# Kernel optimization log

Measured on AMD Instinct MI355X. Metric: run time of the kernel, lower is better.

Reference implementation:

```python
import jax, jax.numpy as jnp
import numpy as np

N = 8192
HID = 64
TAU = 0.8
LAMBDA = 0.5
POS_DENSITY = 0.005


def setup_inputs() -> dict:
    key = jax.random.key(0)
    k1, k2, k3, k4, k5, k6, k7 = jax.random.split(key, 7)
    x1 = jax.random.normal(k1, (N, HID), dtype=jnp.float32)
    x2 = jax.random.normal(k2, (N, HID), dtype=jnp.float32)
    # xavier_uniform with gain=1.414 for square [HID, HID] linears
    limit = 1.414 * np.sqrt(6.0 / (HID + HID))
    W1 = jax.random.uniform(k3, (HID, HID), dtype=jnp.float32, minval=-limit, maxval=limit)
    b1 = jnp.zeros((HID,), dtype=jnp.float32)
    W2 = jax.random.uniform(k4, (HID, HID), dtype=jnp.float32, minval=-limit, maxval=limit)
    b2 = jnp.zeros((HID,), dtype=jnp.float32)
    pm = (jax.random.uniform(k5, (N, N), dtype=jnp.float32) < POS_DENSITY).astype(jnp.float32)
    positive_matrix = jnp.maximum(pm, jnp.eye(N, dtype=jnp.float32))
    return {"x1": x1, "x2": x2, "W1": W1, "b1": b1, "W2": W2, "b2": b2,
            "positive_matrix": positive_matrix}


def _project(x, W1, b1, W2, b2):
    # nn.Linear(hidden, hidden) -> ELU -> nn.Linear(hidden, hidden)
    h = jax.nn.elu(x @ W1.T + b1)
    return h @ W2.T + b2


def _l2norm(z, eps=1e-12):
    # F.normalize(p=2, dim=1): x / max(||x||, eps)
    n = jnp.linalg.norm(z, axis=-1, keepdims=True)
    return z / jnp.maximum(n, eps)


def _sim(z1, z2, tau):
    return jnp.exp((_l2norm(z1) @ _l2norm(z2).T) / tau)  # [N, N]


def _masked_loss(sim_mat, pos):
    row = sim_mat / (jnp.sum(sim_mat, axis=-1, keepdims=True) + 1e-8)
    return -jnp.log(jnp.sum(row * pos, axis=-1) + 1e-8).mean()


def reference(x1, x2, W1, b1, W2, b2, positive_matrix):
    z1 = _project(x1, W1, b1, W2, b2)
    z2 = _project(x2, W1, b1, W2, b2)
    sc_mp = _sim(z1, z2, TAU)
    mp_sc = _sim(z2, z1, TAU)
    sc_loss = _masked_loss(sc_mp, positive_matrix)
    mp_loss = _masked_loss(mp_sc, positive_matrix)
    return sc_loss * LAMBDA + mp_loss * (1.0 - LAMBDA)
```

## Files before the change

kernel.cpp:

```cpp
#include <hip/hip_runtime.h>
#include <hip/hip_bf16.h>

#define N 8192
#define HID 64
#define JC 8

typedef __attribute__((ext_vector_type(4))) float f32x4;
typedef __attribute__((ext_vector_type(8))) __bf16 bf16x8;

#if __has_builtin(__builtin_amdgcn_exp2f)
__device__ __forceinline__ float fast_exp2(float x) {
  return __builtin_amdgcn_exp2f(x);
}
#else
__device__ __forceinline__ float fast_exp2(float x) {
  float r;
  asm volatile("v_exp_f32 %0, %1" : "=v"(r) : "v"(x));
  return r;
}
#endif

__device__ __forceinline__ void gload_lds16(const void* g, float* l) {
  __builtin_amdgcn_global_load_lds(
      (const __attribute__((address_space(1))) void*)g,
      (__attribute__((address_space(3))) void*)l, 16, 0, 0);
}

__global__ __launch_bounds__(256) void proj_kernel(
    const float* __restrict__ x1, const float* __restrict__ x2,
    const float* __restrict__ W1, const float* __restrict__ b1,
    const float* __restrict__ W2, const float* __restrict__ b2,
    __bf16* __restrict__ Z1h, __bf16* __restrict__ Z2h,
    float* __restrict__ stats)
{
  __shared__ __align__(16) float w1s[64*68];
  __shared__ __align__(16) float w2s[64*68];
  __shared__ __align__(16) float xs[4][64];
  __shared__ __align__(16) float hs[4][64];

  const int tid  = threadIdx.x;
  const int lane = tid & 63;
  const int w    = tid >> 6;

  int gtid = blockIdx.x * 256 + tid;
  if (gtid < 4*N) stats[gtid] = 0.f;

  for (int idx = tid; idx < 64*64; idx += 256) {
    int j = idx >> 6, k = idx & 63;
    w1s[j*68+k] = W1[idx];
    w2s[j*68+k] = W2[idx];
  }
  __syncthreads();

  const float bias1 = b1[lane];
  const float bias2 = b2[lane];

  const int wave_global = blockIdx.x * 4 + w;
  #pragma unroll 1
  for (int it = 0; it < 4; ++it) {
    int R = wave_global * 4 + it;
    const float* src; __bf16* dst;
    if (R < N) { src = x1 + (size_t)R*HID;      dst = Z1h + (size_t)R*HID; }
    else       { src = x2 + (size_t)(R-N)*HID;  dst = Z2h + (size_t)(R-N)*HID; }

    float xv = src[lane];
    xs[w][lane] = xv;
    float acc = bias1;
    #pragma unroll
    for (int qq = 0; qq < 16; ++qq) {
      f32x4 xq = *(const f32x4*)&xs[w][qq*4];
      f32x4 wq = *(const f32x4*)&w1s[lane*68 + qq*4];
      acc += xq.x*wq.x + xq.y*wq.y + xq.z*wq.z + xq.w*wq.w;
    }
    float h = acc > 0.f ? acc : expm1f(acc);
    hs[w][lane] = h;
    float acc2 = bias2;
    #pragma unroll
    for (int qq = 0; qq < 16; ++qq) {
      f32x4 hq = *(const f32x4*)&hs[w][qq*4];
      f32x4 wq = *(const f32x4*)&w2s[lane*68 + qq*4];
      acc2 += hq.x*wq.x + hq.y*wq.y + hq.z*wq.z + hq.w*wq.w;
    }
    float z = acc2;
    float ss = z*z;
    #pragma unroll
    for (int m = 1; m < 64; m <<= 1) ss += __shfl_xor(ss, m);
    float inv = 1.0f / fmaxf(sqrtf(ss), 1e-12f);
    dst[lane] = (__bf16)(z * inv);
  }
}

__global__ __launch_bounds__(256, 4) void sim_kernel(
    const __bf16* __restrict__ Z1h, const __bf16* __restrict__ Z2h,
    const float* __restrict__ pos,
    float* __restrict__ rowsum1, float* __restrict__ num1,
    float* __restrict__ rowsum2, float* __restrict__ num2)
{
  __shared__ __align__(16) float zs1[2][2048];
  __shared__ __align__(16) float zs2[2][2048];

  const int tid  = threadIdx.x;
  const int lane = tid & 63;
  const int w    = tid >> 6;
  const int r16  = lane & 15;
  const int q    = lane >> 4;

  const int bi  = blockIdx.x / JC;
  const int jc  = blockIdx.x % JC;
  const int i0  = bi*64 + w*16;

  const __bf16* z1r = Z1h + (size_t)(i0 + r16)*HID + q*8;
  const __bf16* z2r = Z2h + (size_t)(i0 + r16)*HID + q*8;
  const bf16x8 a1lo = *(const bf16x8*)(z1r);
  const bf16x8 a1hi = *(const bf16x8*)(z1r + 32);
  const bf16x8 a2lo = *(const bf16x8*)(z2r);
  const bf16x8 a2hi = *(const bf16x8*)(z2r + 32);

  float s1 = 0.f, n1 = 0.f, s2 = 0.f, n2 = 0.f;

  const int jbeg = jc * (N/JC);
  const float Cexp = 1.8033688011112042f;
  const float* prow = pos + (size_t)(i0 + r16)*N + q*4;

  f32x4 PA0, PA1, PA2, PA3, PB0, PB1, PB2, PB3;

#define STAGEZ(BUF, JJ) { \
    const int r8 = lane >> 3; \
    const int sl = (lane & 7) ^ r8; \
    gload_lds16(Z1h + (size_t)((JJ) + w*16     + r8)*HID + sl*8, &zs1[BUF][(w*16    )*32]); \
    gload_lds16(Z1h + (size_t)((JJ) + w*16 + 8 + r8)*HID + sl*8, &zs1[BUF][(w*16 + 8)*32]); \
    gload_lds16(Z2h + (size_t)((JJ) + w*16     + r8)*HID + sl*8, &zs2[BUF][(w*16    )*32]); \
    gload_lds16(Z2h + (size_t)((JJ) + w*16 + 8 + r8)*HID + sl*8, &zs2[BUF][(w*16 + 8)*32]); \
  }

#define LOADPOS(P, JJ) { \
    P##0 = *(const f32x4*)(prow + (JJ)); \
    P##1 = *(const f32x4*)(prow + (JJ) + 16); \
    P##2 = *(const f32x4*)(prow + (JJ) + 32); \
    P##3 = *(const f32x4*)(prow + (JJ) + 48); \
  }

#define COMPC(BUF, C, CC, PV) { \
    const int R  = (CC) + (C)*16 + r16; \
    const int sw = r16 & 7; \
    bf16x8 b2lo = *(const bf16x8*)&zs2[BUF][R*32 + ((q    ) ^ sw)*4]; \
    bf16x8 b2hi = *(const bf16x8*)&zs2[BUF][R*32 + ((q + 4) ^ sw)*4]; \
    bf16x8 b1lo = *(const bf16x8*)&zs1[BUF][R*32 + ((q    ) ^ sw)*4]; \
    bf16x8 b1hi = *(const bf16x8*)&zs1[BUF][R*32 + ((q + 4) ^ sw)*4]; \
    f32x4 zero4 = {0.f,0.f,0.f,0.f}; \
    f32x4 d1 = __builtin_amdgcn_mfma_f32_16x16x32_bf16(b2lo, a1lo, zero4, 0,0,0); \
    d1       = __builtin_amdgcn_mfma_f32_16x16x32_bf16(b2hi, a1hi, d1,    0,0,0); \
    f32x4 d2 = __builtin_amdgcn_mfma_f32_16x16x32_bf16(b1lo, a2lo, zero4, 0,0,0); \
    d2       = __builtin_amdgcn_mfma_f32_16x16x32_bf16(b1hi, a2hi, d2,    0,0,0); \
    _Pragma("unroll") \
    for (int r = 0; r < 4; ++r) { \
      float e1 = fast_exp2(d1[r] * Cexp); \
      float e2 = fast_exp2(d2[r] * Cexp); \
      s1 += e1; n1 += e1 * PV[r]; \
      s2 += e2; n2 += e2 * PV[r]; \
    } }

#define STEP(BUF, P) { COMPC(BUF,0,0,P##0) COMPC(BUF,1,0,P##1) COMPC(BUF,0,32,P##2) COMPC(BUF,1,32,P##3) }

  STAGEZ(0, jbeg)
  LOADPOS(PA, jbeg)
  __syncthreads();

  #pragma unroll 1
  for (int tp = 0; tp < 7; ++tp) {
    const int t0 = tp*2;
    STAGEZ(1, jbeg + (t0+1)*64)
    LOADPOS(PB, jbeg + (t0+1)*64)
    STEP(0, PA)
    __syncthreads();
    STAGEZ(0, jbeg + (t0+2)*64)
    LOADPOS(PA, jbeg + (t0+2)*64)
    STEP(1, PB)
    __syncthreads();
  }
  STAGEZ(1, jbeg + 15*64)
  LOADPOS(PB, jbeg + 15*64)
  STEP(0, PA)
  __syncthreads();
  STEP(1, PB)

#undef STAGEZ
#undef LOADPOS
#undef COMPC
#undef STEP

  s1 += __shfl_xor(s1, 16); s1 += __shfl_xor(s1, 32);
  n1 += __shfl_xor(n1, 16); n1 += __shfl_xor(n1, 32);
  s2 += __shfl_xor(s2, 16); s2 += __shfl_xor(s2, 32);
  n2 += __shfl_xor(n2, 16); n2 += __shfl_xor(n2, 32);

  if (lane < 16) {
    int row = i0 + r16;
    atomicAdd(&rowsum1[row], s1);
    atomicAdd(&num1[row],    n1);
    atomicAdd(&rowsum2[row], s2);
    atomicAdd(&num2[row],    n2);
  }
}

__global__ __launch_bounds__(1024) void loss_kernel(
    const float* __restrict__ rowsum1, const float* __restrict__ num1,
    const float* __restrict__ rowsum2, const float* __restrict__ num2,
    float* __restrict__ out)
{
  __shared__ float part[16];
  const int tid = threadIdx.x, lane = tid & 63, w = tid >> 6;
  float acc = 0.f;
  for (int i = tid; i < N; i += 1024) {
    float sc = -logf(num1[i]/(rowsum1[i]+1e-8f) + 1e-8f);
    float mp = -logf(num2[i]/(rowsum2[i]+1e-8f) + 1e-8f);
    acc += 0.5f*sc + 0.5f*mp;
  }
  #pragma unroll
  for (int m = 1; m < 64; m <<= 1) acc += __shfl_xor(acc, m);
  if (lane == 0) part[w] = acc;
  __syncthreads();
  if (tid == 0) {
    float t = 0.f;
    #pragma unroll
    for (int k = 0; k < 16; ++k) t += part[k];
    out[0] = t * (1.0f/N);
  }
}

extern "C" void kernel_launch(void* const* d_in, const int* in_sizes, int n_in,
                              void* d_out, int out_size, void* d_ws, size_t ws_size,
                              hipStream_t stream) {
  const float* x1  = (const float*)d_in[0];
  const float* x2  = (const float*)d_in[1];
  const float* W1  = (const float*)d_in[2];
  const float* b1  = (const float*)d_in[3];
  const float* W2  = (const float*)d_in[4];
  const float* b2  = (const float*)d_in[5];
  const float* pos = (const float*)d_in[6];

  char* ws = (char*)d_ws;
  __bf16* Z1h = (__bf16*)ws;
  __bf16* Z2h = (__bf16*)(ws + (size_t)N*HID*sizeof(__bf16));
  size_t zbytes = (size_t)2*N*HID*sizeof(__bf16);
  float* rowsum1 = (float*)(ws + zbytes);
  float* num1    = rowsum1 + N;
  float* rowsum2 = num1 + N;
  float* num2    = rowsum2 + N;

  proj_kernel<<<1024, 256, 0, stream>>>(x1, x2, W1, b1, W2, b2, Z1h, Z2h, rowsum1);
  sim_kernel<<<128*JC, 256, 0, stream>>>(Z1h, Z2h, pos, rowsum1, num1, rowsum2, num2);
  loss_kernel<<<1, 1024, 0, stream>>>(rowsum1, num1, rowsum2, num2, (float*)d_out);
}
```

Baseline: 415.8 us.

## Swap sim kernel tiling to stage j-tile once and loop over i-rows

Each block now loads a single 128-column tile of Z1/Z2 into LDS once and iterates over 512 query rows, reloading A fragments and positive-mask rows per iteration. This removes the double-buffered streaming of Z tiles and the per-step barriers. In exchange it drops the software prefetch of the positive mask, so those global loads are exposed each iteration, and it issues more atomic adds per row.

```diff
diff --git a/kernel.cpp b/kernel.cpp
--- a/kernel.cpp
+++ b/kernel.cpp
@@ -3,7 +3,6 @@
 
 #define N 8192
 #define HID 64
-#define JC 8
 
 typedef __attribute__((ext_vector_type(4))) float f32x4;
 typedef __attribute__((ext_vector_type(8))) __bf16 bf16x8;
@@ -96,8 +95,8 @@
     float* __restrict__ rowsum1, float* __restrict__ num1,
     float* __restrict__ rowsum2, float* __restrict__ num2)
 {
-  __shared__ __align__(16) float zs1[2][2048];
-  __shared__ __align__(16) float zs2[2][2048];
+  __shared__ __align__(16) float zs1[128*32];
+  __shared__ __align__(16) float zs2[128*32];
 
   const int tid  = threadIdx.x;
   const int lane = tid & 63;
@@ -105,48 +104,30 @@
   const int r16  = lane & 15;
   const int q    = lane >> 4;
 
-  const int bi  = blockIdx.x / JC;
-  const int jc  = blockIdx.x % JC;
-  const int i0  = bi*64 + w*16;
-
-  const __bf16* z1r = Z1h + (size_t)(i0 + r16)*HID + q*8;
-  const __bf16* z2r = Z2h + (size_t)(i0 + r16)*HID + q*8;
-  const bf16x8 a1lo = *(const bf16x8*)(z1r);
-  const bf16x8 a1hi = *(const bf16x8*)(z1r + 32);
-  const bf16x8 a2lo = *(const bf16x8*)(z2r);
-  const bf16x8 a2hi = *(const bf16x8*)(z2r + 32);
-
-  float s1 = 0.f, n1 = 0.f, s2 = 0.f, n2 = 0.f;
-
-  const int jbeg = jc * (N/JC);
+  const int jb = (blockIdx.x & 63) * 128;
+  const int ig = (blockIdx.x >> 6) * 512;
+
+  {
+    const int r8 = lane >> 3;
+    const int sl = (lane & 7) ^ r8;
+    #pragma unroll
+    for (int b = 0; b < 4; ++b) {
+      const int row0 = w*32 + b*8;
+      gload_lds16(Z1h + (size_t)(jb + row0 + r8)*HID + sl*8, &zs1[row0*32]);
+      gload_lds16(Z2h + (size_t)(jb + row0 + r8)*HID + sl*8, &zs2[row0*32]);
+    }
+  }
+  __syncthreads();
+
   const float Cexp = 1.8033688011112042f;
-  const float* prow = pos + (size_t)(i0 + r16)*N + q*4;
-
-  f32x4 PA0, PA1, PA2, PA3, PB0, PB1, PB2, PB3;
-
-#define STAGEZ(BUF, JJ) { \
-    const int r8 = lane >> 3; \
-    const int sl = (lane & 7) ^ r8; \
-    gload_lds16(Z1h + (size_t)((JJ) + w*16     + r8)*HID + sl*8, &zs1[BUF][(w*16    )*32]); \
-    gload_lds16(Z1h + (size_t)((JJ) + w*16 + 8 + r8)*HID + sl*8, &zs1[BUF][(w*16 + 8)*32]); \
-    gload_lds16(Z2h + (size_t)((JJ) + w*16     + r8)*HID + sl*8, &zs2[BUF][(w*16    )*32]); \
-    gload_lds16(Z2h + (size_t)((JJ) + w*16 + 8 + r8)*HID + sl*8, &zs2[BUF][(w*16 + 8)*32]); \
-  }
-
-#define LOADPOS(P, JJ) { \
-    P##0 = *(const f32x4*)(prow + (JJ)); \
-    P##1 = *(const f32x4*)(prow + (JJ) + 16); \
-    P##2 = *(const f32x4*)(prow + (JJ) + 32); \
-    P##3 = *(const f32x4*)(prow + (JJ) + 48); \
-  }
-
-#define COMPC(BUF, C, CC, PV) { \
-    const int R  = (CC) + (C)*16 + r16; \
+
+#define COMPC(S, PV) { \
+    const int R  = (S)*16 + r16; \
     const int sw = r16 & 7; \
-    bf16x8 b2lo = *(const bf16x8*)&zs2[BUF][R*32 + ((q    ) ^ sw)*4]; \
-    bf16x8 b2hi = *(const bf16x8*)&zs2[BUF][R*32 + ((q + 4) ^ sw)*4]; \
-    bf16x8 b1lo = *(const bf16x8*)&zs1[BUF][R*32 + ((q    ) ^ sw)*4]; \
-    bf16x8 b1hi = *(const bf16x8*)&zs1[BUF][R*32 + ((q + 4) ^ sw)*4]; \
+    bf16x8 b2lo = *(const bf16x8*)&zs2[R*32 + ((q    ) ^ sw)*4]; \
+    bf16x8 b2hi = *(const bf16x8*)&zs2[R*32 + ((q + 4) ^ sw)*4]; \
+    bf16x8 b1lo = *(const bf16x8*)&zs1[R*32 + ((q    ) ^ sw)*4]; \
+    bf16x8 b1hi = *(const bf16x8*)&zs1[R*32 + ((q + 4) ^ sw)*4]; \
     f32x4 zero4 = {0.f,0.f,0.f,0.f}; \
     f32x4 d1 = __builtin_amdgcn_mfma_f32_16x16x32_bf16(b2lo, a1lo, zero4, 0,0,0); \
     d1       = __builtin_amdgcn_mfma_f32_16x16x32_bf16(b2hi, a1hi, d1,    0,0,0); \
@@ -160,47 +141,46 @@
       s2 += e2; n2 += e2 * PV[r]; \
     } }
 
-#define STEP(BUF, P) { COMPC(BUF,0,0,P##0) COMPC(BUF,1,0,P##1) COMPC(BUF,0,32,P##2) COMPC(BUF,1,32,P##3) }
-
-  STAGEZ(0, jbeg)
-  LOADPOS(PA, jbeg)
-  __syncthreads();
-
   #pragma unroll 1
-  for (int tp = 0; tp < 7; ++tp) {
-    const int t0 = tp*2;
-    STAGEZ(1, jbeg + (t0+1)*64)
-    LOADPOS(PB, jbeg + (t0+1)*64)
-    STEP(0, PA)
-    __syncthreads();
-    STAGEZ(0, jbeg + (t0+2)*64)
-    LOADPOS(PA, jbeg + (t0+2)*64)
-    STEP(1, PB)
-    __syncthreads();
-  }
-  STAGEZ(1, jbeg + 15*64)
-  LOADPOS(PB, jbeg + 15*64)
-  STEP(0, PA)
-  __syncthreads();
-  STEP(1, PB)
-
-#undef STAGEZ
-#undef LOADPOS
+  for (int it = 0; it < 8; ++it) {
+    const int i0 = ig + it*64 + w*16;
+
+    const __bf16* z1r = Z1h + (size_t)(i0 + r16)*HID + q*8;
+    const __bf16* z2r = Z2h + (size_t)(i0 + r16)*HID + q*8;
+    const bf16x8 a1lo = *(const bf16x8*)(z1r);
+    const bf16x8 a1hi = *(const bf16x8*)(z1r + 32);
+    const bf16x8 a2lo = *(const bf16x8*)(z2r);
+    const bf16x8 a2hi = *(const bf16x8*)(z2r + 32);
+
+    const float* prow = pos + (size_t)(i0 + r16)*N + jb + q*4;
+    const f32x4 P0 = *(const f32x4*)(prow);
+    const f32x4 P1 = *(const f32x4*)(prow + 16);
+    const f32x4 P2 = *(const f32x4*)(prow + 32);
+    const f32x4 P3 = *(const f32x4*)(prow + 48);
+    const f32x4 P4 = *(const f32x4*)(prow + 64);
+    const f32x4 P5 = *(const f32x4*)(prow + 80);
+    const f32x4 P6 = *(const f32x4*)(prow + 96);
+    const f32x4 P7 = *(const f32x4*)(prow + 112);
+
+    float s1 = 0.f, n1 = 0.f, s2 = 0.f, n2 = 0.f;
+
+    COMPC(0, P0) COMPC(1, P1) COMPC(2, P2) COMPC(3, P3)
+    COMPC(4, P4) COMPC(5, P5) COMPC(6, P6) COMPC(7, P7)
+
+    s1 += __shfl_xor(s1, 16); s1 += __shfl_xor(s1, 32);
+    n1 += __shfl_xor(n1, 16); n1 += __shfl_xor(n1, 32);
+    s2 += __shfl_xor(s2, 16); s2 += __shfl_xor(s2, 32);
+    n2 += __shfl_xor(n2, 16); n2 += __shfl_xor(n2, 32);
+
+    if (lane < 16) {
+      int row = i0 + r16;
+      atomicAdd(&rowsum1[row], s1);
+      atomicAdd(&num1[row],    n1);
+      atomicAdd(&rowsum2[row], s2);
+      atomicAdd(&num2[row],    n2);
+    }
+  }
 #undef COMPC
-#undef STEP
-
-  s1 += __shfl_xor(s1, 16); s1 += __shfl_xor(s1, 32);
-  n1 += __shfl_xor(n1, 16); n1 += __shfl_xor(n1, 32);
-  s2 += __shfl_xor(s2, 16); s2 += __shfl_xor(s2, 32);
-  n2 += __shfl_xor(n2, 16); n2 += __shfl_xor(n2, 32);
-
-  if (lane < 16) {
-    int row = i0 + r16;
-    atomicAdd(&rowsum1[row], s1);
-    atomicAdd(&num1[row],    n1);
-    atomicAdd(&rowsum2[row], s2);
-    atomicAdd(&num2[row],    n2);
-  }
 }
 
 __global__ __launch_bounds__(1024) void loss_kernel(
@@ -249,6 +229,6 @@
   float* num2    = rowsum2 + N;
 
   proj_kernel<<<1024, 256, 0, stream>>>(x1, x2, W1, b1, W2, b2, Z1h, Z2h, rowsum1);
-  sim_kernel<<<128*JC, 256, 0, stream>>>(Z1h, Z2h, pos, rowsum1, num1, rowsum2, num2);
+  sim_kernel<<<1024, 256, 0, stream>>>(Z1h, Z2h, pos, rowsum1, num1, rowsum2, num2);
   loss_kernel<<<1, 1024, 0, stream>>>(rowsum1, num1, rowsum2, num2, (float*)d_out);
 }
```

Measured after the change: 461.7 us. +11.0%, slower.
